# Performance work log

Hardware: AMD Instinct MI355X
Metric: run time of the kernel (lower is better)

The kernel has to match this reference:

```python
import jax, jax.numpy as jnp
import numpy as np

N = 100000   # nodes
E = 800000   # edges
H = 64       # hidden_channels (also input feature dim via lazy Linear)
OUT = 2      # out_channels
G = 64       # graphs in batch
EPS = 1e-5   # BatchNorm eps
N_PRE, N_CONV, N_POST = 3, 6, 3


def setup_inputs() -> dict:
    key = jax.random.key(0)
    ks = jax.random.split(key, 20)
    s = 0.1
    inp = {
        "x": jax.random.normal(ks[0], (N, H), jnp.float32),
        "edge_index": jax.random.randint(ks[1], (2, E), 0, N, dtype=jnp.int64),
        "batch": jnp.sort(jax.random.randint(ks[2], (N,), 0, G, dtype=jnp.int64)),
        # pre-processing MLP + BN params
        "pre_W": jax.random.normal(ks[3], (N_PRE, H, H), jnp.float32) * s,
        "pre_b": jax.random.normal(ks[4], (N_PRE, H), jnp.float32) * s,
        "pre_g": jnp.ones((N_PRE, H), jnp.float32),
        "pre_beta": jnp.zeros((N_PRE, H), jnp.float32),
        # GCNConv params (weight + bias per layer)
        "conv_W": jax.random.normal(ks[5], (N_CONV, H, H), jnp.float32) * s,
        "conv_b": jax.random.normal(ks[6], (N_CONV, H), jnp.float32) * s,
        # post-processing MLP + BN params
        "post_W": jax.random.normal(ks[7], (N_POST, H, H), jnp.float32) * s,
        "post_b": jax.random.normal(ks[8], (N_POST, H), jnp.float32) * s,
        "post_g": jnp.ones((N_POST, H), jnp.float32),
        "post_beta": jnp.zeros((N_POST, H), jnp.float32),
        # final head: H->H, H->H, H->OUT
        "fin_W0": jax.random.normal(ks[9], (H, H), jnp.float32) * s,
        "fin_b0": jax.random.normal(ks[10], (H,), jnp.float32) * s,
        "fin_W1": jax.random.normal(ks[11], (H, H), jnp.float32) * s,
        "fin_b1": jax.random.normal(ks[12], (H,), jnp.float32) * s,
        "fin_W2": jax.random.normal(ks[13], (H, OUT), jnp.float32) * s,
        "fin_b2": jax.random.normal(ks[14], (OUT,), jnp.float32) * s,
    }
    return inp


def _bn(h, g, b):
    # BatchNorm1d, training mode: biased batch statistics over node dim
    m = h.mean(0)
    v = h.var(0)
    return (h - m) * jax.lax.rsqrt(v + EPS) * g + b


def _gcn(h, src, dst, dinv, W, b):
    # PyG GCNConv: h' = D^-1/2 (A+I) D^-1/2 (h W) + b, sum-aggregated at dst
    hw = h @ W                                   # [N,H]
    norm = dinv[src] * dinv[dst]                 # [E]
    agg = jax.ops.segment_sum(hw[src] * norm[:, None], dst, num_segments=N)
    agg = agg + hw * (dinv * dinv)[:, None]      # self-loop contribution
    return agg + b


def reference(x, edge_index, batch, pre_W, pre_b, pre_g, pre_beta,
              conv_W, conv_b, post_W, post_b, post_g, post_beta,
              fin_W0, fin_b0, fin_W1, fin_b1, fin_W2, fin_b2):
    src, dst = edge_index[0], edge_index[1]
    # gcn_norm degree with self-loops (in-degree at dst), edge_weight = 1
    deg = jax.ops.segment_sum(jnp.ones((E,), x.dtype), dst, num_segments=N) + 1.0
    dinv = jax.lax.rsqrt(deg)

    h = x
    # pre-processing: Linear -> BN, relu except last
    for i in range(N_PRE):
        h = _bn(h @ pre_W[i] + pre_b[i], pre_g[i], pre_beta[i])
        if i != N_PRE - 1:
            h = jax.nn.relu(h)
    # GCNConv stack with residual adds
    for i in range(N_CONV):
        h = _gcn(h, src, dst, dinv, conv_W[i], conv_b[i]) + h
        if i != N_CONV - 1:
            h = jax.nn.relu(h)
    # post-processing: Linear -> BN, relu except last
    for i in range(N_POST):
        h = _bn(h @ post_W[i] + post_b[i], post_g[i], post_beta[i])
        if i != N_POST - 1:
            h = jax.nn.relu(h)
    # global_mean_pool over graphs
    counts = jax.ops.segment_sum(jnp.ones((N,), h.dtype), batch, num_segments=G)
    pooled = jax.ops.segment_sum(h, batch, num_segments=G) / jnp.maximum(counts, 1.0)[:, None]
    # final head (dropout is identity in eval)
    z = jax.nn.relu(pooled @ fin_W0 + fin_b0)
    z = jax.nn.relu(z @ fin_W1 + fin_b1)
    return z @ fin_W2 + fin_b2
```

## Files before the change

kernel.cpp:

```cpp
#include <hip/hip_runtime.h>

#define N_NODES 100000
#define N_EDGES 800000
#define HID 64
#define NGRAPH 64
#define OUTC 2
#define BN_EPS 1e-5f
#define NSCAN_BLK ((N_NODES + 255) / 256)
#define GEMM_BLK ((N_NODES + 63) / 64)
#define POOL_SUB 16

typedef __attribute__((ext_vector_type(8))) short bf16x8;
typedef __attribute__((ext_vector_type(4))) float f32x4;

__device__ __forceinline__ unsigned short f2bf(float f) {
    unsigned int u = __float_as_uint(f);
    u = (u + 0x7FFFu + ((u >> 16) & 1u)) >> 16;
    return (unsigned short)u;
}

template <int IN_MODE, bool ADD_BIAS, bool ROW_SCALE, bool STATS, bool OUT_BF16>
__global__ __launch_bounds__(256) void k_gemm(const float* __restrict__ X,
                                              const float* __restrict__ W,
                                              const float* __restrict__ bias,
                                              const float* __restrict__ dinv,
                                              const float* __restrict__ scsh,
                                              void* __restrict__ Yv,
                                              float* __restrict__ partial, int n) {
    __shared__ __align__(16) unsigned short sXb[64][72];
    __shared__ __align__(16) unsigned short sWT[64][72];
    __shared__ float sDinv[64];
    const int tid  = threadIdx.x;
    const int row0 = blockIdx.x * 64;

    #pragma unroll
    for (int i = tid; i < 1024; i += 256) {
        int k = i >> 4, c4 = (i & 15) << 2;
        float4 w = *reinterpret_cast<const float4*>(&W[k * 64 + c4]);
        sWT[c4 + 0][k] = f2bf(w.x);
        sWT[c4 + 1][k] = f2bf(w.y);
        sWT[c4 + 2][k] = f2bf(w.z);
        sWT[c4 + 3][k] = f2bf(w.w);
    }
    #pragma unroll
    for (int f = tid; f < 1024; f += 256) {
        int r = f >> 4, c4 = (f & 15) << 2;
        float4 v = make_float4(0.f, 0.f, 0.f, 0.f);
        if (row0 + r < n)
            v = *reinterpret_cast<const float4*>(&X[(size_t)(row0 + r) * HID + c4]);
        if (IN_MODE >= 1) {
            float4 sc = *reinterpret_cast<const float4*>(&scsh[c4]);
            float4 sh = *reinterpret_cast<const float4*>(&scsh[64 + c4]);
            v.x = v.x * sc.x + sh.x; v.y = v.y * sc.y + sh.y;
            v.z = v.z * sc.z + sh.z; v.w = v.w * sc.w + sh.w;
            if (IN_MODE == 2) {
                v.x = fmaxf(v.x, 0.f); v.y = fmaxf(v.y, 0.f);
                v.z = fmaxf(v.z, 0.f); v.w = fmaxf(v.w, 0.f);
            }
        }
        sXb[r][c4 + 0] = f2bf(v.x);
        sXb[r][c4 + 1] = f2bf(v.y);
        sXb[r][c4 + 2] = f2bf(v.z);
        sXb[r][c4 + 3] = f2bf(v.w);
    }
    if (ROW_SCALE && tid < 64)
        sDinv[tid] = (row0 + tid < n) ? dinv[row0 + tid] : 0.f;
    __syncthreads();

    const int lane = tid & 63;
    const int wv   = tid >> 6;
    const int cl   = lane & 15;
    const int kg   = lane >> 4;
    const int col  = (wv << 4) + cl;

    const f32x4 zero = {0.f, 0.f, 0.f, 0.f};
    f32x4 acc[4];
    #pragma unroll
    for (int m = 0; m < 4; ++m) acc[m] = zero;

    #pragma unroll
    for (int k0 = 0; k0 < 64; k0 += 32) {
        bf16x8 bfrag = *reinterpret_cast<const bf16x8*>(&sWT[col][k0 + (kg << 3)]);
        #pragma unroll
        for (int m = 0; m < 4; ++m) {
            bf16x8 afrag = *reinterpret_cast<const bf16x8*>(&sXb[(m << 4) + cl][k0 + (kg << 3)]);
            acc[m] = __builtin_amdgcn_mfma_f32_16x16x32_bf16(afrag, bfrag, acc[m], 0, 0, 0);
        }
    }

    const float bb = ADD_BIAS ? bias[col] : 0.f;
    float colS = 0.f, colQ = 0.f;
    #pragma unroll
    for (int m = 0; m < 4; ++m) {
        #pragma unroll
        for (int j = 0; j < 4; ++j) {
            int rl = (m << 4) + (kg << 2) + j;
            int r  = row0 + rl;
            if (r < n) {
                float s = ROW_SCALE ? sDinv[rl] : 1.f;
                float o = acc[m][j] * s + bb;
                if (OUT_BF16)
                    ((unsigned short*)Yv)[(size_t)r * HID + col] = f2bf(o);
                else
                    ((float*)Yv)[(size_t)r * HID + col] = o;
                if (STATS) { colS += o; colQ += o * o; }
            }
        }
    }
    if (STATS) {
        colS += __shfl_xor(colS, 16); colQ += __shfl_xor(colQ, 16);
        colS += __shfl_xor(colS, 32); colQ += __shfl_xor(colQ, 32);
        if (kg == 0) {
            partial[blockIdx.x * 128 + col]      = colS;
            partial[blockIdx.x * 128 + 64 + col] = colQ;
        }
    }
}

__global__ __launch_bounds__(256) void k_statsfin(const float* __restrict__ partial,
                                                  const float* __restrict__ g,
                                                  const float* __restrict__ beta,
                                                  float* __restrict__ scsh, int n) {
    int c = blockIdx.x, t = threadIdx.x;
    float S = 0.f, Q = 0.f;
    for (int b = t; b < GEMM_BLK; b += 256) {
        S += partial[b * 128 + c];
        Q += partial[b * 128 + 64 + c];
    }
    __shared__ float ss[256], sq[256];
    ss[t] = S; sq[t] = Q;
    __syncthreads();
    for (int off = 128; off > 0; off >>= 1) {
        if (t < off) { ss[t] += ss[t + off]; sq[t] += sq[t + off]; }
        __syncthreads();
    }
    if (t == 0) {
        float nf = (float)n;
        float m  = ss[0] / nf;
        float v  = sq[0] / nf - m * m;
        float sc = rsqrtf(v + BN_EPS) * g[c];
        scsh[c]      = sc;
        scsh[64 + c] = beta[c] - m * sc;
    }
}

__global__ __launch_bounds__(256) void k_deg(const int* __restrict__ dst,
                                             int* __restrict__ indeg) {
    int e = blockIdx.x * 256 + threadIdx.x;
    if (e < N_EDGES) atomicAdd(&indeg[dst[e]], 1);
}

__global__ __launch_bounds__(256) void k_scanpart(const int* __restrict__ indeg,
                                                  int* __restrict__ bsum) {
    __shared__ int s[256];
    int i = blockIdx.x * 256 + threadIdx.x;
    s[threadIdx.x] = (i < N_NODES) ? indeg[i] : 0;
    __syncthreads();
    for (int off = 128; off > 0; off >>= 1) {
        if (threadIdx.x < off) s[threadIdx.x] += s[threadIdx.x + off];
        __syncthreads();
    }
    if (threadIdx.x == 0) bsum[blockIdx.x] = s[0];
}

__global__ __launch_bounds__(512) void k_scanmid(int* __restrict__ bsum, int nblk) {
    __shared__ int s[512];
    int t = threadIdx.x;
    int v = (t < nblk) ? bsum[t] : 0;
    s[t] = v;
    __syncthreads();
    for (int off = 1; off < 512; off <<= 1) {
        int x = (t >= off) ? s[t - off] : 0;
        __syncthreads();
        s[t] += x;
        __syncthreads();
    }
    if (t < nblk) bsum[t] = s[t] - v;
}

__global__ __launch_bounds__(256) void k_scanfinal(const int* __restrict__ indeg,
                                                   const int* __restrict__ bsum,
                                                   int* __restrict__ rowptr) {
    __shared__ int s[256];
    int t = threadIdx.x;
    int i = blockIdx.x * 256 + t;
    int v = (i < N_NODES) ? indeg[i] : 0;
    s[t] = v;
    __syncthreads();
    for (int off = 1; off < 256; off <<= 1) {
        int x = (t >= off) ? s[t - off] : 0;
        __syncthreads();
        s[t] += x;
        __syncthreads();
    }
    if (i < N_NODES) rowptr[i] = bsum[blockIdx.x] + s[t] - v;
    if (i == 0) rowptr[N_NODES] = N_EDGES;
}

__global__ __launch_bounds__(256) void k_dinv(const int* __restrict__ indeg,
                                              float* __restrict__ dinv) {
    int i = blockIdx.x * 256 + threadIdx.x;
    if (i < N_NODES) dinv[i] = rsqrtf((float)indeg[i] + 1.f);
}

__global__ __launch_bounds__(256) void k_fill(const int* __restrict__ src,
                                              const int* __restrict__ dst,
                                              const int* __restrict__ rowptr,
                                              int* __restrict__ indeg,
                                              int* __restrict__ colidx) {
    int e = blockIdx.x * 256 + threadIdx.x;
    if (e >= N_EDGES) return;
    int d = dst[e];
    int pos = rowptr[d] + (atomicSub(&indeg[d], 1) - 1);
    colidx[pos] = src[e];
}

template <int IN_MODE, bool RELU>
__global__ __launch_bounds__(256) void k_gather(const int* __restrict__ rowptr,
                                                const int* __restrict__ colidx,
                                                const unsigned short* __restrict__ HWb,
                                                const float* __restrict__ Hin,
                                                const float* __restrict__ dinv,
                                                const float* __restrict__ bias,
                                                const float* __restrict__ scsh,
                                                float* __restrict__ Out) {
    int d = blockIdx.x * 4 + (threadIdx.x >> 6);
    if (d >= N_NODES) return;
    const int lane = threadIdx.x & 63;
    const int slot = lane >> 3;
    const int c8   = (lane & 7) << 3;
    const int j0 = rowptr[d], j1 = rowptr[d + 1];

    float acc[8];
    #pragma unroll
    for (int k = 0; k < 8; ++k) acc[k] = 0.f;

    if (slot == 7) {
        uint4 v = *reinterpret_cast<const uint4*>(&HWb[(size_t)d * HID + c8]);
        acc[0] += __uint_as_float(v.x << 16);
        acc[1] += __uint_as_float(v.x & 0xFFFF0000u);
        acc[2] += __uint_as_float(v.y << 16);
        acc[3] += __uint_as_float(v.y & 0xFFFF0000u);
        acc[4] += __uint_as_float(v.z << 16);
        acc[5] += __uint_as_float(v.z & 0xFFFF0000u);
        acc[6] += __uint_as_float(v.w << 16);
        acc[7] += __uint_as_float(v.w & 0xFFFF0000u);
    }
    for (int j = j0 + slot; j < j1; j += 8) {
        int s = colidx[j];
        uint4 v = *reinterpret_cast<const uint4*>(&HWb[(size_t)s * HID + c8]);
        acc[0] += __uint_as_float(v.x << 16);
        acc[1] += __uint_as_float(v.x & 0xFFFF0000u);
        acc[2] += __uint_as_float(v.y << 16);
        acc[3] += __uint_as_float(v.y & 0xFFFF0000u);
        acc[4] += __uint_as_float(v.z << 16);
        acc[5] += __uint_as_float(v.z & 0xFFFF0000u);
        acc[6] += __uint_as_float(v.w << 16);
        acc[7] += __uint_as_float(v.w & 0xFFFF0000u);
    }
    #pragma unroll
    for (int m = 8; m < 64; m <<= 1) {
        #pragma unroll
        for (int k = 0; k < 8; ++k) acc[k] += __shfl_xor(acc[k], m);
    }

    if (slot == 0) {
        float4 h0 = *reinterpret_cast<const float4*>(&Hin[(size_t)d * HID + c8]);
        float4 h1 = *reinterpret_cast<const float4*>(&Hin[(size_t)d * HID + c8 + 4]);
        if (IN_MODE == 1) {
            float4 sc0 = *reinterpret_cast<const float4*>(&scsh[c8]);
            float4 sc1 = *reinterpret_cast<const float4*>(&scsh[c8 + 4]);
            float4 sh0 = *reinterpret_cast<const float4*>(&scsh[64 + c8]);
            float4 sh1 = *reinterpret_cast<const float4*>(&scsh[64 + c8 + 4]);
            h0.x = h0.x * sc0.x + sh0.x; h0.y = h0.y * sc0.y + sh0.y;
            h0.z = h0.z * sc0.z + sh0.z; h0.w = h0.w * sc0.w + sh0.w;
            h1.x = h1.x * sc1.x + sh1.x; h1.y = h1.y * sc1.y + sh1.y;
            h1.z = h1.z * sc1.z + sh1.z; h1.w = h1.w * sc1.w + sh1.w;
        }
        float di = dinv[d];
        float4 b0 = *reinterpret_cast<const float4*>(&bias[c8]);
        float4 b1 = *reinterpret_cast<const float4*>(&bias[c8 + 4]);
        float4 o0, o1;
        o0.x = acc[0] * di + b0.x + h0.x;
        o0.y = acc[1] * di + b0.y + h0.y;
        o0.z = acc[2] * di + b0.z + h0.z;
        o0.w = acc[3] * di + b0.w + h0.w;
        o1.x = acc[4] * di + b1.x + h1.x;
        o1.y = acc[5] * di + b1.y + h1.y;
        o1.z = acc[6] * di + b1.z + h1.z;
        o1.w = acc[7] * di + b1.w + h1.w;
        if (RELU) {
            o0.x = fmaxf(o0.x, 0.f); o0.y = fmaxf(o0.y, 0.f);
            o0.z = fmaxf(o0.z, 0.f); o0.w = fmaxf(o0.w, 0.f);
            o1.x = fmaxf(o1.x, 0.f); o1.y = fmaxf(o1.y, 0.f);
            o1.z = fmaxf(o1.z, 0.f); o1.w = fmaxf(o1.w, 0.f);
        }
        *reinterpret_cast<float4*>(&Out[(size_t)d * HID + c8])     = o0;
        *reinterpret_cast<float4*>(&Out[(size_t)d * HID + c8 + 4]) = o1;
    }
}

__device__ __forceinline__ int lowerb(const int* __restrict__ b, int n, int v) {
    int lo = 0, hi = n;
    while (lo < hi) { int m = (lo + hi) >> 1; if (b[m] < v) lo = m + 1; else hi = m; }
    return lo;
}

__global__ __launch_bounds__(256) void k_pool1(const float* __restrict__ Y,
                                               const int* __restrict__ batch,
                                               float* __restrict__ partial2) {
    int g  = blockIdx.x >> 4;
    int sb = blockIdx.x & 15;
    int tid = threadIdx.x, col = tid & 63, rg = tid >> 6;
    int lo = lowerb(batch, N_NODES, g);
    int hi = lowerb(batch, N_NODES, g + 1);
    int cnt = hi - lo;
    int st = lo + (int)(((long long)cnt * sb) >> 4);
    int en = lo + (int)(((long long)cnt * (sb + 1)) >> 4);
    float s = 0.f;
    for (int r = st + rg; r < en; r += 4) s += Y[(size_t)r * HID + col];
    __shared__ float ls[4][64];
    ls[rg][col] = s;
    __syncthreads();
    if (tid < 64)
        partial2[(size_t)blockIdx.x * 64 + tid] =
            ls[0][tid] + ls[1][tid] + ls[2][tid] + ls[3][tid];
}

__global__ __launch_bounds__(64) void k_pool2(const float* __restrict__ partial2,
                                              const int* __restrict__ batch,
                                              const float* __restrict__ scsh,
                                              float* __restrict__ pooled) {
    int g = blockIdx.x, c = threadIdx.x;
    float S = 0.f;
    #pragma unroll
    for (int sb = 0; sb < POOL_SUB; ++sb)
        S += partial2[(size_t)(g * POOL_SUB + sb) * 64 + c];
    int lo = lowerb(batch, N_NODES, g);
    int hi = lowerb(batch, N_NODES, g + 1);
    int cnt = hi - lo;
    float out = 0.f;
    if (cnt > 0) {
        float mean = S / (float)cnt;
        out = mean * scsh[c] + scsh[64 + c];
    }
    pooled[g * 64 + c] = out;
}

__global__ __launch_bounds__(256) void k_final(const float* __restrict__ pooled,
                                               const float* __restrict__ W0,
                                               const float* __restrict__ b0,
                                               const float* __restrict__ W1,
                                               const float* __restrict__ b1,
                                               const float* __restrict__ W2,
                                               const float* __restrict__ b2,
                                               float* __restrict__ out) {
    __shared__ float P[64][65];
    __shared__ float Z[64][65];
    int tid = threadIdx.x;
    for (int i = tid; i < NGRAPH * HID; i += 256) P[i >> 6][i & 63] = pooled[i];
    __syncthreads();
    for (int t = 0; t < 16; ++t) {
        int o = tid + 256 * t; int r = o >> 6, c = o & 63;
        float acc = b0[c];
        #pragma unroll 8
        for (int k = 0; k < 64; ++k) acc += P[r][k] * W0[k * 64 + c];
        Z[r][c] = fmaxf(acc, 0.f);
    }
    __syncthreads();
    for (int t = 0; t < 16; ++t) {
        int o = tid + 256 * t; int r = o >> 6, c = o & 63;
        float acc = b1[c];
        #pragma unroll 8
        for (int k = 0; k < 64; ++k) acc += Z[r][k] * W1[k * 64 + c];
        P[r][c] = fmaxf(acc, 0.f);
    }
    __syncthreads();
    if (tid < NGRAPH * OUTC) {
        int r = tid >> 1, c = tid & 1;
        float acc = b2[c];
        #pragma unroll 8
        for (int k = 0; k < 64; ++k) acc += P[r][k] * W2[k * OUTC + c];
        out[tid] = acc;
    }
}

extern "C" void kernel_launch(void* const* d_in, const int* in_sizes, int n_in,
                              void* d_out, int out_size, void* d_ws, size_t ws_size,
                              hipStream_t stream) {
    const float* x        = (const float*)d_in[0];
    const int*   ei       = (const int*)d_in[1];
    const int*   batch    = (const int*)d_in[2];
    const float* pre_W    = (const float*)d_in[3];
    const float* pre_b    = (const float*)d_in[4];
    const float* pre_g    = (const float*)d_in[5];
    const float* pre_beta = (const float*)d_in[6];
    const float* conv_W   = (const float*)d_in[7];
    const float* conv_b   = (const float*)d_in[8];
    const float* post_W   = (const float*)d_in[9];
    const float* post_b   = (const float*)d_in[10];
    const float* post_g   = (const float*)d_in[11];
    const float* post_beta= (const float*)d_in[12];
    const float* fW0 = (const float*)d_in[13];
    const float* fb0 = (const float*)d_in[14];
    const float* fW1 = (const float*)d_in[15];
    const float* fb1 = (const float*)d_in[16];
    const float* fW2 = (const float*)d_in[17];
    const float* fb2 = (const float*)d_in[18];
    float* out = (float*)d_out;

    const size_t NH = (size_t)N_NODES * HID;
    float* ws       = (float*)d_ws;
    float* A        = ws;
    float* B        = A + NH;
    float* C        = B + NH;
    float* dinv     = C + NH;
    float* partial  = dinv + N_NODES;
    float* scsh     = partial + (size_t)GEMM_BLK*128;
    float* pooled   = scsh + 6 * 128;
    float* partial2 = pooled + NGRAPH * HID;
    int*   indeg    = (int*)(partial2 + NGRAPH * POOL_SUB * 64);
    int*   rowptr   = indeg + N_NODES;
    int*   colidx   = rowptr + N_NODES + 1;
    int*   bsum     = colidx + N_EDGES;
    unsigned short* HWb = (unsigned short*)B;

    const int* srcp = ei;
    const int* dstp = ei + N_EDGES;

    const int gEdge  = (N_EDGES + 255) / 256;
    const int gNode  = (N_NODES + 255) / 256;
    const int gNode4 = (N_NODES + 3) / 4;

    hipMemsetAsync(indeg, 0, N_NODES * sizeof(int), stream);
    k_deg<<<gEdge, 256, 0, stream>>>(dstp, indeg);
    k_scanpart<<<NSCAN_BLK, 256, 0, stream>>>(indeg, bsum);
    k_scanmid<<<1, 512, 0, stream>>>(bsum, NSCAN_BLK);
    k_scanfinal<<<NSCAN_BLK, 256, 0, stream>>>(indeg, bsum, rowptr);
    k_dinv<<<gNode, 256, 0, stream>>>(indeg, dinv);
    k_fill<<<gEdge, 256, 0, stream>>>(srcp, dstp, rowptr, indeg, colidx);

    k_gemm<0, true, false, true, false><<<GEMM_BLK, 256, 0, stream>>>(x, pre_W, pre_b, nullptr, nullptr, A, partial, N_NODES);
    k_statsfin<<<64, 256, 0, stream>>>(partial, pre_g, pre_beta, scsh + 0 * 128, N_NODES);

    k_gemm<2, true, false, true, false><<<GEMM_BLK, 256, 0, stream>>>(A, pre_W + 4096, pre_b + 64, nullptr, scsh + 0 * 128, (float*)(C), partial, N_NODES);
    k_statsfin<<<64, 256, 0, stream>>>(partial, pre_g + 64, pre_beta + 64, scsh + 1 * 128, N_NODES);

    k_gemm<2, true, false, true, false><<<GEMM_BLK, 256, 0, stream>>>(C, pre_W + 2 * 4096, pre_b + 128, nullptr, scsh + 1 * 128, A, partial, N_NODES);
    k_statsfin<<<64, 256, 0, stream>>>(partial, pre_g + 128, pre_beta + 128, scsh + 2 * 128, N_NODES);

    for (int i = 0; i < 6; ++i) {
        const float* in = (i & 1) ? C : A;
        float*     outb = (i & 1) ? A : C;
        const float* Wl = conv_W + i * 4096;
        const float* bl = conv_b + i * 64;
        if (i == 0)
            k_gemm<1, false, true, false, true><<<GEMM_BLK, 256, 0, stream>>>(in, Wl, nullptr, dinv, scsh + 2 * 128, HWb, nullptr, N_NODES);
        else
            k_gemm<0, false, true, false, true><<<GEMM_BLK, 256, 0, stream>>>(in, Wl, nullptr, dinv, nullptr, HWb, nullptr, N_NODES);

        if (i == 0)
            k_gather<1, true ><<<gNode4, 256, 0, stream>>>(rowptr, colidx, HWb, in, dinv, bl, scsh + 2 * 128, outb);
        else if (i != 5)
            k_gather<0, true ><<<gNode4, 256, 0, stream>>>(rowptr, colidx, HWb, in, dinv, bl, nullptr, outb);
        else
            k_gather<0, false><<<gNode4, 256, 0, stream>>>(rowptr, colidx, HWb, in, dinv, bl, nullptr, outb);
    }

    k_gemm<0, true, false, true, false><<<GEMM_BLK, 256, 0, stream>>>(A, post_W, post_b, nullptr, nullptr, C, partial, N_NODES);
    k_statsfin<<<64, 256, 0, stream>>>(partial, post_g, post_beta, scsh + 3 * 128, N_NODES);

    k_gemm<2, true, false, true, false><<<GEMM_BLK, 256, 0, stream>>>(C, post_W + 4096, post_b + 64, nullptr, scsh + 3 * 128, A, partial, N_NODES);
    k_statsfin<<<64, 256, 0, stream>>>(partial, post_g + 64, post_beta + 64, scsh + 4 * 128, N_NODES);

    k_gemm<2, true, false, true, false><<<GEMM_BLK, 256, 0, stream>>>(A, post_W + 2 * 4096, post_b + 128, nullptr, scsh + 4 * 128, C, partial, N_NODES);
    k_statsfin<<<64, 256, 0, stream>>>(partial, post_g + 128, post_beta + 128, scsh + 5 * 128, N_NODES);

    k_pool1<<<NGRAPH * POOL_SUB, 256, 0, stream>>>(C, batch, partial2);
    k_pool2<<<NGRAPH, 64, 0, stream>>>(partial2, batch, scsh + 5 * 128, pooled);
    k_final<<<1, 256, 0, stream>>>(pooled, fW0, fb0, fW1, fb1, fW2, fb2, out);
}
```

Measured before the change: 571.1 us.

## Store all intermediate activations as bf16 and fuse small kernels

Every intermediate activation buffer (GEMM outputs, gather outputs, the residual input) is now stored in bf16 instead of fp32, which halves global memory traffic between the many bandwidth-bound stages. The dinv computation is folded into the scan-final kernel, and the pool2 kernel is merged into the final head kernel, removing two launches. The cost is more rounding of the residual stream and BN inputs, which could change accuracy.

```diff
diff --git a/kernel.cpp b/kernel.cpp
--- a/kernel.cpp
+++ b/kernel.cpp
@@ -18,14 +18,19 @@
     u = (u + 0x7FFFu + ((u >> 16) & 1u)) >> 16;
     return (unsigned short)u;
 }
-
-template <int IN_MODE, bool ADD_BIAS, bool ROW_SCALE, bool STATS, bool OUT_BF16>
-__global__ __launch_bounds__(256) void k_gemm(const float* __restrict__ X,
+__device__ __forceinline__ float bflo(unsigned int u) { return __uint_as_float(u << 16); }
+__device__ __forceinline__ float bfhi(unsigned int u) { return __uint_as_float(u & 0xFFFF0000u); }
+__device__ __forceinline__ unsigned int bfpack(float a, float b) {
+    return (unsigned int)f2bf(a) | ((unsigned int)f2bf(b) << 16);
+}
+
+template <int IN_MODE, bool IN_FP32, bool ADD_BIAS, bool ROW_SCALE, bool STATS>
+__global__ __launch_bounds__(256) void k_gemm(const void* __restrict__ Xv,
                                               const float* __restrict__ W,
                                               const float* __restrict__ bias,
                                               const float* __restrict__ dinv,
                                               const float* __restrict__ scsh,
-                                              void* __restrict__ Yv,
+                                              unsigned short* __restrict__ Y,
                                               float* __restrict__ partial, int n) {
     __shared__ __align__(16) unsigned short sXb[64][72];
     __shared__ __align__(16) unsigned short sWT[64][72];
@@ -42,26 +47,53 @@
         sWT[c4 + 2][k] = f2bf(w.z);
         sWT[c4 + 3][k] = f2bf(w.w);
     }
-    #pragma unroll
-    for (int f = tid; f < 1024; f += 256) {
-        int r = f >> 4, c4 = (f & 15) << 2;
-        float4 v = make_float4(0.f, 0.f, 0.f, 0.f);
-        if (row0 + r < n)
-            v = *reinterpret_cast<const float4*>(&X[(size_t)(row0 + r) * HID + c4]);
-        if (IN_MODE >= 1) {
-            float4 sc = *reinterpret_cast<const float4*>(&scsh[c4]);
-            float4 sh = *reinterpret_cast<const float4*>(&scsh[64 + c4]);
-            v.x = v.x * sc.x + sh.x; v.y = v.y * sc.y + sh.y;
-            v.z = v.z * sc.z + sh.z; v.w = v.w * sc.w + sh.w;
-            if (IN_MODE == 2) {
-                v.x = fmaxf(v.x, 0.f); v.y = fmaxf(v.y, 0.f);
-                v.z = fmaxf(v.z, 0.f); v.w = fmaxf(v.w, 0.f);
+    if (IN_FP32) {
+        const float* X = (const float*)Xv;
+        #pragma unroll
+        for (int f = tid; f < 1024; f += 256) {
+            int r = f >> 4, c4 = (f & 15) << 2;
+            float4 v = make_float4(0.f, 0.f, 0.f, 0.f);
+            if (row0 + r < n)
+                v = *reinterpret_cast<const float4*>(&X[(size_t)(row0 + r) * HID + c4]);
+            if (IN_MODE >= 1) {
+                float4 sc = *reinterpret_cast<const float4*>(&scsh[c4]);
+                float4 sh = *reinterpret_cast<const float4*>(&scsh[64 + c4]);
+                v.x = v.x * sc.x + sh.x; v.y = v.y * sc.y + sh.y;
+                v.z = v.z * sc.z + sh.z; v.w = v.w * sc.w + sh.w;
+                if (IN_MODE == 2) {
+                    v.x = fmaxf(v.x, 0.f); v.y = fmaxf(v.y, 0.f);
+                    v.z = fmaxf(v.z, 0.f); v.w = fmaxf(v.w, 0.f);
+                }
             }
-        }
-        sXb[r][c4 + 0] = f2bf(v.x);
-        sXb[r][c4 + 1] = f2bf(v.y);
-        sXb[r][c4 + 2] = f2bf(v.z);
-        sXb[r][c4 + 3] = f2bf(v.w);
+            sXb[r][c4 + 0] = f2bf(v.x);
+            sXb[r][c4 + 1] = f2bf(v.y);
+            sXb[r][c4 + 2] = f2bf(v.z);
+            sXb[r][c4 + 3] = f2bf(v.w);
+        }
+    } else {
+        const unsigned short* X = (const unsigned short*)Xv;
+        #pragma unroll
+        for (int f = tid; f < 512; f += 256) {
+            int r = f >> 3, c8 = (f & 7) << 3;
+            uint4 u = make_uint4(0u, 0u, 0u, 0u);
+            if (row0 + r < n)
+                u = *reinterpret_cast<const uint4*>(&X[(size_t)(row0 + r) * HID + c8]);
+            if (IN_MODE >= 1) {
+                float v[8];
+                v[0] = bflo(u.x); v[1] = bfhi(u.x);
+                v[2] = bflo(u.y); v[3] = bfhi(u.y);
+                v[4] = bflo(u.z); v[5] = bfhi(u.z);
+                v[6] = bflo(u.w); v[7] = bfhi(u.w);
+                #pragma unroll
+                for (int k = 0; k < 8; ++k) {
+                    v[k] = v[k] * scsh[c8 + k] + scsh[64 + c8 + k];
+                    if (IN_MODE == 2) v[k] = fmaxf(v[k], 0.f);
+                }
+                u.x = bfpack(v[0], v[1]); u.y = bfpack(v[2], v[3]);
+                u.z = bfpack(v[4], v[5]); u.w = bfpack(v[6], v[7]);
+            }
+            *reinterpret_cast<uint4*>(&sXb[r][c8]) = u;
+        }
     }
     if (ROW_SCALE && tid < 64)
         sDinv[tid] = (row0 + tid < n) ? dinv[row0 + tid] : 0.f;
@@ -99,10 +131,7 @@
             if (r < n) {
                 float s = ROW_SCALE ? sDinv[rl] : 1.f;
                 float o = acc[m][j] * s + bb;
-                if (OUT_BF16)
-                    ((unsigned short*)Yv)[(size_t)r * HID + col] = f2bf(o);
-                else
-                    ((float*)Yv)[(size_t)r * HID + col] = o;
+                Y[(size_t)r * HID + col] = f2bf(o);
                 if (STATS) { colS += o; colQ += o * o; }
             }
         }
@@ -180,7 +209,8 @@
 
 __global__ __launch_bounds__(256) void k_scanfinal(const int* __restrict__ indeg,
                                                    const int* __restrict__ bsum,
-                                                   int* __restrict__ rowptr) {
+                                                   int* __restrict__ rowptr,
+                                                   float* __restrict__ dinv) {
     __shared__ int s[256];
     int t = threadIdx.x;
     int i = blockIdx.x * 256 + t;
@@ -193,14 +223,11 @@
         s[t] += x;
         __syncthreads();
     }
-    if (i < N_NODES) rowptr[i] = bsum[blockIdx.x] + s[t] - v;
+    if (i < N_NODES) {
+        rowptr[i] = bsum[blockIdx.x] + s[t] - v;
+        dinv[i]   = rsqrtf((float)v + 1.f);
+    }
     if (i == 0) rowptr[N_NODES] = N_EDGES;
-}
-
-__global__ __launch_bounds__(256) void k_dinv(const int* __restrict__ indeg,
-                                              float* __restrict__ dinv) {
-    int i = blockIdx.x * 256 + threadIdx.x;
-    if (i < N_NODES) dinv[i] = rsqrtf((float)indeg[i] + 1.f);
 }
 
 __global__ __launch_bounds__(256) void k_fill(const int* __restrict__ src,
@@ -219,11 +246,11 @@
 __global__ __launch_bounds__(256) void k_gather(const int* __restrict__ rowptr,
                                                 const int* __restrict__ colidx,
                                                 const unsigned short* __restrict__ HWb,
-                                                const float* __restrict__ Hin,
+                                                const unsigned short* __restrict__ Hin,
                                                 const float* __restrict__ dinv,
                                                 const float* __restrict__ bias,
                                                 const float* __restrict__ scsh,
-                                                float* __restrict__ Out) {
+                                                unsigned short* __restrict__ Out) {
     int d = blockIdx.x * 4 + (threadIdx.x >> 6);
     if (d >= N_NODES) return;
     const int lane = threadIdx.x & 63;
@@ -237,26 +264,18 @@
 
     if (slot == 7) {
         uint4 v = *reinterpret_cast<const uint4*>(&HWb[(size_t)d * HID + c8]);
-        acc[0] += __uint_as_float(v.x << 16);
-        acc[1] += __uint_as_float(v.x & 0xFFFF0000u);
-        acc[2] += __uint_as_float(v.y << 16);
-        acc[3] += __uint_as_float(v.y & 0xFFFF0000u);
-        acc[4] += __uint_as_float(v.z << 16);
-        acc[5] += __uint_as_float(v.z & 0xFFFF0000u);
-        acc[6] += __uint_as_float(v.w << 16);
-        acc[7] += __uint_as_float(v.w & 0xFFFF0000u);
+        acc[0] += bflo(v.x); acc[1] += bfhi(v.x);
+        acc[2] += bflo(v.y); acc[3] += bfhi(v.y);
+        acc[4] += bflo(v.z); acc[5] += bfhi(v.z);
+        acc[6] += bflo(v.w); acc[7] += bfhi(v.w);
     }
     for (int j = j0 + slot; j < j1; j += 8) {
         int s = colidx[j];
         uint4 v = *reinterpret_cast<const uint4*>(&HWb[(size_t)s * HID + c8]);
-        acc[0] += __uint_as_float(v.x << 16);
-        acc[1] += __uint_as_float(v.x & 0xFFFF0000u);
-        acc[2] += __uint_as_float(v.y << 16);
-        acc[3] += __uint_as_float(v.y & 0xFFFF0000u);
-        acc[4] += __uint_as_float(v.z << 16);
-        acc[5] += __uint_as_float(v.z & 0xFFFF0000u);
-        acc[6] += __uint_as_float(v.w << 16);
-        acc[7] += __uint_as_float(v.w & 0xFFFF0000u);
+        acc[0] += bflo(v.x); acc[1] += bfhi(v.x);
+        acc[2] += bflo(v.y); acc[3] += bfhi(v.y);
+        acc[4] += bflo(v.z); acc[5] += bfhi(v.z);
+        acc[6] += bflo(v.w); acc[7] += bfhi(v.w);
     }
     #pragma unroll
     for (int m = 8; m < 64; m <<= 1) {
@@ -265,38 +284,28 @@
     }
 
     if (slot == 0) {
-        float4 h0 = *reinterpret_cast<const float4*>(&Hin[(size_t)d * HID + c8]);
-        float4 h1 = *reinterpret_cast<const float4*>(&Hin[(size_t)d * HID + c8 + 4]);
+        uint4 hv = *reinterpret_cast<const uint4*>(&Hin[(size_t)d * HID + c8]);
+        float h[8];
+        h[0] = bflo(hv.x); h[1] = bfhi(hv.x);
+        h[2] = bflo(hv.y); h[3] = bfhi(hv.y);
+        h[4] = bflo(hv.z); h[5] = bfhi(hv.z);
+        h[6] = bflo(hv.w); h[7] = bfhi(hv.w);
         if (IN_MODE == 1) {
-            float4 sc0 = *reinterpret_cast<const float4*>(&scsh[c8]);
-            float4 sc1 = *reinterpret_cast<const float4*>(&scsh[c8 + 4]);
-            float4 sh0 = *reinterpret_cast<const float4*>(&scsh[64 + c8]);
-            float4 sh1 = *reinterpret_cast<const float4*>(&scsh[64 + c8 + 4]);
-            h0.x = h0.x * sc0.x + sh0.x; h0.y = h0.y * sc0.y + sh0.y;
-            h0.z = h0.z * sc0.z + sh0.z; h0.w = h0.w * sc0.w + sh0.w;
-            h1.x = h1.x * sc1.x + sh1.x; h1.y = h1.y * sc1.y + sh1.y;
-            h1.z = h1.z * sc1.z + sh1.z; h1.w = h1.w * sc1.w + sh1.w;
+            #pragma unroll
+            for (int k = 0; k < 8; ++k)
+                h[k] = h[k] * scsh[c8 + k] + scsh[64 + c8 + k];
         }
         float di = dinv[d];
-        float4 b0 = *reinterpret_cast<const float4*>(&bias[c8]);
-        float4 b1 = *reinterpret_cast<const float4*>(&bias[c8 + 4]);
-        float4 o0, o1;
-        o0.x = acc[0] * di + b0.x + h0.x;
-        o0.y = acc[1] * di + b0.y + h0.y;
-        o0.z = acc[2] * di + b0.z + h0.z;
-        o0.w = acc[3] * di + b0.w + h0.w;
-        o1.x = acc[4] * di + b1.x + h1.x;
-        o1.y = acc[5] * di + b1.y + h1.y;
-        o1.z = acc[6] * di + b1.z + h1.z;
-        o1.w = acc[7] * di + b1.w + h1.w;
-        if (RELU) {
-            o0.x = fmaxf(o0.x, 0.f); o0.y = fmaxf(o0.y, 0.f);
-            o0.z = fmaxf(o0.z, 0.f); o0.w = fmaxf(o0.w, 0.f);
-            o1.x = fmaxf(o1.x, 0.f); o1.y = fmaxf(o1.y, 0.f);
-            o1.z = fmaxf(o1.z, 0.f); o1.w = fmaxf(o1.w, 0.f);
-        }
-        *reinterpret_cast<float4*>(&Out[(size_t)d * HID + c8])     = o0;
-        *reinterpret_cast<float4*>(&Out[(size_t)d * HID + c8 + 4]) = o1;
+        float o[8];
+        #pragma unroll
+        for (int k = 0; k < 8; ++k) {
+            o[k] = acc[k] * di + bias[c8 + k] + h[k];
+            if (RELU) o[k] = fmaxf(o[k], 0.f);
+        }
+        uint4 ov;
+        ov.x = bfpack(o[0], o[1]); ov.y = bfpack(o[2], o[3]);
+        ov.z = bfpack(o[4], o[5]); ov.w = bfpack(o[6], o[7]);
+        *reinterpret_cast<uint4*>(&Out[(size_t)d * HID + c8]) = ov;
     }
 }
 
@@ -306,7 +315,7 @@
     return lo;
 }
 
-__global__ __launch_bounds__(256) void k_pool1(const float* __restrict__ Y,
+__global__ __launch_bounds__(256) void k_pool1(const unsigned short* __restrict__ Y,
                                                const int* __restrict__ batch,
                                                float* __restrict__ partial2) {
     int g  = blockIdx.x >> 4;
@@ -318,7 +327,8 @@
     int st = lo + (int)(((long long)cnt * sb) >> 4);
     int en = lo + (int)(((long long)cnt * (sb + 1)) >> 4);
     float s = 0.f;
-    for (int r = st + rg; r < en; r += 4) s += Y[(size_t)r * HID + col];
+    for (int r = st + rg; r < en; r += 4)
+        s += bflo((unsigned int)Y[(size_t)r * HID + col]);
     __shared__ float ls[4][64];
     ls[rg][col] = s;
     __syncthreads();
@@ -327,27 +337,9 @@
             ls[0][tid] + ls[1][tid] + ls[2][tid] + ls[3][tid];
 }
 
-__global__ __launch_bounds__(64) void k_pool2(const float* __restrict__ partial2,
-                                              const int* __restrict__ batch,
-                                              const float* __restrict__ scsh,
-                                              float* __restrict__ pooled) {
-    int g = blockIdx.x, c = threadIdx.x;
-    float S = 0.f;
-    #pragma unroll
-    for (int sb = 0; sb < POOL_SUB; ++sb)
-        S += partial2[(size_t)(g * POOL_SUB + sb) * 64 + c];
-    int lo = lowerb(batch, N_NODES, g);
-    int hi = lowerb(batch, N_NODES, g + 1);
-    int cnt = hi - lo;
-    float out = 0.f;
-    if (cnt > 0) {
-        float mean = S / (float)cnt;
-        out = mean * scsh[c] + scsh[64 + c];
-    }
-    pooled[g * 64 + c] = out;
-}
-
-__global__ __launch_bounds__(256) void k_final(const float* __restrict__ pooled,
+__global__ __launch_bounds__(256) void k_final(const float* __restrict__ partial2,
+                                               const int* __restrict__ batch,
+                                               const float* __restrict__ scsh,
                                                const float* __restrict__ W0,
                                                const float* __restrict__ b0,
                                                const float* __restrict__ W1,
@@ -358,7 +350,19 @@
     __shared__ float P[64][65];
     __shared__ float Z[64][65];
     int tid = threadIdx.x;
-    for (int i = tid; i < NGRAPH * HID; i += 256) P[i >> 6][i & 63] = pooled[i];
+    for (int i = tid; i < NGRAPH * HID; i += 256) {
+        int g = i >> 6, c = i & 63;
+        float S = 0.f;
+        #pragma unroll
+        for (int sb = 0; sb < POOL_SUB; ++sb)
+            S += partial2[(size_t)(g * POOL_SUB + sb) * 64 + c];
+        int lo = lowerb(batch, N_NODES, g);
+        int hi = lowerb(batch, N_NODES, g + 1);
+        int cnt = hi - lo;
+        float v = 0.f;
+        if (cnt > 0) v = (S / (float)cnt) * scsh[c] + scsh[64 + c];
+        P[g][c] = v;
+    }
     __syncthreads();
     for (int t = 0; t < 16; ++t) {
         int o = tid + 256 * t; int r = o >> 6, c = o & 63;
@@ -417,66 +421,65 @@
     float* dinv     = C + NH;
     float* partial  = dinv + N_NODES;
     float* scsh     = partial + (size_t)GEMM_BLK*128;
-    float* pooled   = scsh + 6 * 128;
-    float* partial2 = pooled + NGRAPH * HID;
+    float* partial2 = scsh + 6 * 128;
     int*   indeg    = (int*)(partial2 + NGRAPH * POOL_SUB * 64);
     int*   rowptr   = indeg + N_NODES;
     int*   colidx   = rowptr + N_NODES + 1;
     int*   bsum     = colidx + N_EDGES;
-    unsigned short* HWb = (unsigned short*)B;
+    unsigned short* Ab  = (unsigned short*)A;
+    unsigned short* Bb  = (unsigned short*)B;
+    unsigned short* Cb  = (unsigned short*)C;
 
     const int* srcp = ei;
     const int* dstp = ei + N_EDGES;
 
     const int gEdge  = (N_EDGES + 255) / 256;
-    const int gNode  = (N_NODES + 255) / 256;
     const int gNode4 = (N_NODES + 3) / 4;
 
     hipMemsetAsync(indeg, 0, N_NODES * sizeof(int), stream);
     k_deg<<<gEdge, 256, 0, stream>>>(dstp, indeg);
     k_scanpart<<<NSCAN_BLK, 256, 0, stream>>>(indeg, bsum);
     k_scanmid<<<1, 512, 0, stream>>>(bsum, NSCAN_BLK);
-    k_scanfinal<<<NSCAN_BLK, 256, 0, stream>>>(indeg, bsum, rowptr);
-    k_dinv<<<gNode, 256, 0, stream>>>(indeg, dinv);
+    k_scanfinal<<<NSCAN_BLK, 256, 0, stream>>>(indeg, bsum, rowptr, dinv);
     k_fill<<<gEdge, 256, 0, stream>>>(srcp, dstp, rowptr, indeg, colidx);
 
-    k_gemm<0, true, false, true, false><<<GEMM_BLK, 256, 0, stream>>>(x, pre_W, pre_b, nullptr, nullptr, A, partial, N_NODES);
+    k_gemm<0, true,  true, false, true><<<GEMM_BLK, 256, 0, stream>>>(x, pre_W, pre_b, nullptr, nullptr, Ab, partial, N_NODES);
     k_statsfin<<<64, 256, 0, stream>>>(partial, pre_g, pre_beta, scsh + 0 * 128, N_NODES);
 
-    k_gemm<2, true, false, true, false><<<GEMM_BLK, 256, 0, stream>>>(A, pre_W + 4096, pre_b + 64, nullptr, scsh + 0 * 128, (float*)(C), partial, N_NODES);
+    k_gemm<2, false, true, false, true><<<GEMM_BLK, 256, 0, stream>>>(Ab, pre_W + 4096, pre_b + 64, nullptr, scsh + 0 * 128, Cb, partial, N_NODES);
     k_statsfin<<<64, 256, 0, stream>>>(partial, pre_g + 64, pre_beta + 64, scsh + 1 * 128, N_NODES);
 
-    k_gemm<2, true, false, true, false><<<GEMM_BLK, 256, 0, stream>>>(C, pre_W + 2 * 4096, pre_b + 128, nullptr, scsh + 1 * 128, A, partial, N_NODES);
+    k_gemm<2, false, true, false, true><<<GEMM_BLK, 256, 0, stream>>>(Cb, pre_W + 2 * 4096, pre_b + 128, nullptr, scsh + 1 * 128, Ab, partial, N_NODES);
     k_statsfin<<<64, 256, 0, stream>>>(partial, pre_g + 128, pre_beta + 128, scsh + 2 * 128, N_NODES);
 
     for (int i = 0; i < 6; ++i) {
-        const float* in = (i & 1) ? C : A;
-        float*     outb = (i & 1) ? A : C;
+        const unsigned short* in = (i & 1) ? Cb : Ab;
+        unsigned short*     outb = (i & 1) ? Ab : Cb;
         const float* Wl = conv_W + i * 4096;
         const float* bl = conv_b + i * 64;
         if (i == 0)
-            k_gemm<1, false, true, false, true><<<GEMM_BLK, 256, 0, stream>>>(in, Wl, nullptr, dinv, scsh + 2 * 128, HWb, nullptr, N_NODES);
+            k_gemm<1, false, false, true, false><<<GEMM_BLK, 256, 0, stream>>>(in, Wl, nullptr, dinv, scsh + 2 * 128, Bb, nullptr, N_NODES);
         else
-            k_gemm<0, false, true, false, true><<<GEMM_BLK, 256, 0, stream>>>(in, Wl, nullptr, dinv, nullptr, HWb, nullptr, N_NODES);
+            k_gemm<0, false, false, true, false><<<GEMM_BLK, 256, 0, stream>>>(in, Wl, nullptr, dinv, nullptr, Bb, nullptr, N_NODES);
 
         if (i == 0)
-            k_gather<1, true ><<<gNode4, 256, 0, stream>>>(rowptr, colidx, HWb, in, dinv, bl, scsh + 2 * 128, outb);
+            k_gather<1, true ><<<gNode4, 256, 0, stream>>>(rowptr, colidx, Bb, in, dinv, bl, scsh + 2 * 128, outb);
         else if (i != 5)
-            k_gather<0, true ><<<gNode4, 256, 0, stream>>>(rowptr, colidx, HWb, in, dinv, bl, nullptr, outb);
+            k_gather<0, true ><<<gNode4, 256, 0, stream>>>(rowptr, colidx, Bb, in, dinv, bl, nullptr, outb);
         else
-            k_gather<0, false><<<gNode4, 256, 0, stream>>>(rowptr, colidx, HWb, in, dinv, bl, nullptr, outb);
-    }
-
-    k_gemm<0, true, false, true, false><<<GEMM_BLK, 256, 0, stream>>>(A, post_W, post_b, nullptr, nullptr, C, partial, N_NODES);
+            k_gather<0, false><<<gNode4, 256, 0, stream>>>(rowptr, colidx, Bb, in, dinv, bl, nullptr, outb);
+    }
+
+    k_gemm<0, false, true, false, true><<<GEMM_BLK, 256, 0, stream>>>(Ab, post_W, post_b, nullptr, nullptr, Cb, partial, N_NODES);
     k_statsfin<<<64, 256, 0, stream>>>(partial, post_g, post_beta, scsh + 3 * 128, N_NODES);
 
-    k_gemm<2, true, false, true, false><<<GEMM_BLK, 256, 0, stream>>>(C, post_W + 4096, post_b + 64, nullptr, scsh + 3 * 128, A, partial, N_NODES);
+    k_gemm<2, false, true, false, true><<<GEMM_BLK, 256, 0, stream>>>(Cb, post_W + 4096, post_b + 64, nullptr, scsh + 3 * 128, Ab, partial, N_NODES);
     k_statsfin<<<64, 256, 0, stream>>>(partial, post_g + 64, post_beta + 64, scsh + 4 * 128, N_NODES);
 
-    k_gemm<2, true, false, true, false><<<GEMM_BLK, 256, 0, stream>>>(A, post_W + 2 * 4096, post_b + 128, nullptr, scsh + 4 * 128, C, partial, N_NODES);
+    k_gemm<2, false, true, false, true><<<GEMM_BLK, 256, 0, stream>>>(Ab, post_W + 2 * 4096, post_b + 128, nullptr, scsh + 4 * 128, Cb, partial, N_NODES);
     k_statsfin<<<64, 256, 0, stream>>>(partial, post_g + 128, post_beta + 128, scsh + 5 * 128, N_NODES);
 
-    k_pool1<<<NGRAPH * POOL_SUB, 256, 0, stream>>>(C, batch, partial2);
-    k_pool2<<<NGRAPH, 64, 0, stream>>>(partial2, batch, scsh + 5 * 128, pooled);
-    k_final<<<1, 256, 0, stream>>>(pooled, fW0, fb0, fW1, fb1, fW2, fb2, out);
-}
+    k_pool1<<<NGRAPH * POOL_SUB, 256, 0, stream>>>(Cb, batch, partial2);
+    k_final<<<1, 256, 0, stream>>>(partial2, batch, scsh + 5 * 128,
+                                   fW0, fb0, fW1, fb1, fW2, fb2, out);
+}
```

Result: slower. 652.5 us (+14.3%).
